# Performance work log

Measured on AMD Instinct MI355X. Metric: run time of the kernel, lower is better.

## Reference

```python
import jax, jax.numpy as jnp
import numpy as np

N_NODES = 100000
N_EDGES = 1600000
IN_F = 256
OUT_F = 64
ORDER = 3


def setup_inputs() -> dict:
    key = jax.random.key(0)
    k1, k2, k3, k4, k5 = jax.random.split(key, 5)
    x = jax.random.normal(k1, (N_NODES, IN_F), dtype=jnp.float32)
    # Linear params (torch nn.Linear: out = x @ W.T + b)
    W = jax.random.normal(k2, (OUT_F, IN_F), dtype=jnp.float32) * (1.0 / np.sqrt(IN_F))
    b = jnp.zeros((OUT_F,), dtype=jnp.float32)
    edge_src = jax.random.randint(k3, (N_EDGES,), 0, N_NODES, dtype=jnp.int32)
    edge_dst = jax.random.randint(k4, (N_EDGES,), 0, N_NODES, dtype=jnp.int32)
    # normalized-adjacency-like positive edge weights
    edge_weight = jax.random.uniform(k5, (N_EDGES,), dtype=jnp.float32) * 0.1
    return {"x": x, "W": W, "b": b, "edge_src": edge_src,
            "edge_dst": edge_dst, "edge_weight": edge_weight}


def reference(x, W, b, edge_src, edge_dst, edge_weight):
    # SGC: linear projection, then `order` hops of sparse adjacency matmul.
    out = x @ W.T + b  # [N, OUT_F]
    for _ in range(ORDER):
        # spmm: out[dst] += w_e * out[src] over all edges (COO)
        msgs = out[edge_src] * edge_weight[:, None]  # [E, OUT_F]
        out = jax.ops.segment_sum(msgs, edge_dst, num_segments=N_NODES)
    return out
```

## Files before the change

### kernel.cpp

```cpp
#include <hip/hip_runtime.h>

#define IN_F 256
#define OUT_F 64
#define BKT_BITS 8
#define BKT_NODES 256
#define BKT_CAP 6656
#define SRC_BITS 18
#define SRC_MASK 0x3FFFF
#define BIN_BLOCKS 256

typedef __attribute__((ext_vector_type(8))) short short8;
typedef __attribute__((ext_vector_type(4))) float floatx4;
typedef __attribute__((ext_vector_type(4))) int intx4;

static __device__ __forceinline__ short f2bf_rne(float f) {
    unsigned u = __float_as_uint(f);
    unsigned r = (u + 0x7fffu + ((u >> 16) & 1u)) >> 16;
    return (short)r;
}
static __device__ __forceinline__ float bf2f(short s) {
    return __uint_as_float(((unsigned)(unsigned short)s) << 16);
}
static __device__ __forceinline__ float bfu2f(unsigned short s) {
    return __uint_as_float(((unsigned)s) << 16);
}

__global__ __launch_bounds__(1024) void bin_kernel(const int* __restrict__ src,
                                                   const int* __restrict__ dst,
                                                   const float* __restrict__ w,
                                                   int* __restrict__ bkt_cnt,
                                                   int2* __restrict__ binned, int E, int nbkt) {
    __shared__ int h[512];
    int t = threadIdx.x;
    if (t < 512) h[t] = 0;
    __syncthreads();
    int ce = (E + BIN_BLOCKS - 1) / BIN_BLOCKS;
    int beg = blockIdx.x * ce;
    int end = min(E, beg + ce);
    for (int e = beg + t; e < end; e += 1024)
        atomicAdd(&h[__builtin_nontemporal_load(dst + e) >> BKT_BITS], 1);
    __syncthreads();
    int c = (t < 512) ? h[t] : 0;
    int r = 0;
    if (t < nbkt && c) r = atomicAdd(&bkt_cnt[t], c);
    __syncthreads();
    if (t < 512) h[t] = r;
    __syncthreads();
    for (int e = beg + t; e < end; e += 1024) {
        int d = dst[e];
        int bb = d >> BKT_BITS;
        int pos = atomicAdd(&h[bb], 1);
        binned[(size_t)bb * BKT_CAP + pos] =
            make_int2(((d & (BKT_NODES - 1)) << SRC_BITS) | src[e], __float_as_int(w[e]));
    }
}

__global__ __launch_bounds__(256) void build_bucket_kernel(const int2* __restrict__ binned,
                                                           const int* __restrict__ bkt_cnt,
                                                           int2* __restrict__ bego,
                                                           int2* __restrict__ edges,
                                                           int N) {
    __shared__ int h[BKT_NODES];
    __shared__ int ssum[256];
    int t = threadIdx.x;
    int b = blockIdx.x;
    h[t] = 0;
    __syncthreads();
    int cntb = bkt_cnt[b];
    const int2* bsrc = binned + (size_t)b * BKT_CAP;
    for (int e = t; e < cntb; e += 256) atomicAdd(&h[bsrc[e].x >> SRC_BITS], 1);
    __syncthreads();
    int c = h[t];
    int p = (c + 7) & ~7;
    ssum[t] = p;
    __syncthreads();
    for (int off = 1; off < 256; off <<= 1) {
        int v = (t >= off) ? ssum[t - off] : 0;
        __syncthreads();
        ssum[t] += v;
        __syncthreads();
    }
    int base = b * BKT_CAP + (t > 0 ? ssum[t - 1] : 0);
    int node = (b << BKT_BITS) + t;
    if (node < N) bego[node] = make_int2(base, base + p);
    __syncthreads();
    h[t] = base;
    __syncthreads();
    for (int e = t; e < cntb; e += 256) {
        int2 v = bsrc[e];
        int pos = atomicAdd(&h[v.x >> SRC_BITS], 1);
        edges[pos] = make_int2(v.x & SRC_MASK, v.y);
    }
    __syncthreads();
    for (int k = h[t]; k < base + p; ++k) edges[k] = make_int2(0, 0);
}

__global__ void prep_kernel(const float* __restrict__ W,
                            short* __restrict__ bh, short* __restrict__ bl,
                            int* __restrict__ bkt_cnt, int nbkt) {
    int blk = blockIdx.x;
    if (blk >= 8) {
        int i = (blk - 8) * 256 + threadIdx.x;
        if (i < nbkt) bkt_cnt[i] = 0;
        return;
    }
    int t = blk * 256 + threadIdx.x;
    int combo = t >> 6;
    int lane = t & 63;
    int s = combo >> 2;
    int tO = combo & 3;
    int n = 16 * tO + (lane & 15);
    int k0 = 32 * s + (lane >> 4) * 8;
    const float* src = W + (size_t)n * IN_F + k0;
    short* dh = bh + (size_t)t * 8;
    short* dl = bl + (size_t)t * 8;
#pragma unroll
    for (int j = 0; j < 8; ++j) {
        float v = src[j];
        short h = f2bf_rne(v);
        dh[j] = h;
        dl[j] = f2bf_rne(v - bf2f(h));
    }
}

__global__ __launch_bounds__(256) void gemm_kernel(const float* __restrict__ x,
                                                   const short8* __restrict__ bh,
                                                   const short8* __restrict__ bl,
                                                   const float* __restrict__ b,
                                                   unsigned short* __restrict__ obf, int N) {
    int lane = threadIdx.x & 63;
    int wid = threadIdx.x >> 6;
    int node0 = blockIdx.x * 64 + wid * 16;
    if (node0 >= N) return;
    if (node0 + 16 > N) node0 = N - 16;
    int m = lane & 15;
    int q = lane >> 4;

    const floatx4* xr = (const floatx4*)(x + (size_t)(node0 + m) * IN_F) + q * 2;

    floatx4 acc[4];
#pragma unroll
    for (int tO = 0; tO < 4; ++tO) acc[tO] = (floatx4){0.f, 0.f, 0.f, 0.f};

#pragma unroll
    for (int s = 0; s < 8; ++s) {
        floatx4 v0 = __builtin_nontemporal_load(xr + s * 8);
        floatx4 v1 = __builtin_nontemporal_load(xr + s * 8 + 1);
        float vv[8] = {v0[0], v0[1], v0[2], v0[3], v1[0], v1[1], v1[2], v1[3]};
        short8 ah, al;
#pragma unroll
        for (int j = 0; j < 8; ++j) {
            short h = f2bf_rne(vv[j]);
            ah[j] = h;
            al[j] = f2bf_rne(vv[j] - bf2f(h));
        }
#pragma unroll
        for (int tO = 0; tO < 4; ++tO) {
            short8 wh = bh[(s * 4 + tO) * 64 + lane];
            short8 wl = bl[(s * 4 + tO) * 64 + lane];
            acc[tO] = __builtin_amdgcn_mfma_f32_16x16x32_bf16(ah, wh, acc[tO], 0, 0, 0);
            acc[tO] = __builtin_amdgcn_mfma_f32_16x16x32_bf16(al, wh, acc[tO], 0, 0, 0);
            acc[tO] = __builtin_amdgcn_mfma_f32_16x16x32_bf16(ah, wl, acc[tO], 0, 0, 0);
        }
    }

#pragma unroll
    for (int tO = 0; tO < 4; ++tO) {
        float bias = b[16 * tO + m];
#pragma unroll
        for (int r = 0; r < 4; ++r) {
            obf[(size_t)(node0 + q * 4 + r) * OUT_F + 16 * tO + m] =
                (unsigned short)f2bf_rne(acc[tO][r] + bias);
        }
    }
}

#define GATHER_Q(NB)                                                                     \
    {                                                                                    \
        intx4 Q[NB];                                                                     \
        float v[2 * NB];                                                                 \
        _Pragma("unroll") for (int j = 0; j < NB; ++j) Q[j] = eq[j];                     \
        _Pragma("unroll") for (int j = 0; j < NB; ++j) {                                 \
            v[2 * j]     = bfu2f(in[(size_t)Q[j][0] * OUT_F + lane]);                    \
            v[2 * j + 1] = bfu2f(in[(size_t)Q[j][2] * OUT_F + lane]);                    \
        }                                                                                \
        _Pragma("unroll") for (int j = 0; j < NB; ++j) {                                 \
            acc = fmaf(__int_as_float(Q[j][1]), v[2 * j], acc);                          \
            acc = fmaf(__int_as_float(Q[j][3]), v[2 * j + 1], acc);                      \
        }                                                                                \
    }

static __device__ __forceinline__ float spmm_node(const int2* __restrict__ edges,
                                                  const unsigned short* __restrict__ in,
                                                  int lane, int e, int end) {
    float acc = 0.f;
    int deg = end - e;
    const intx4* eq = (const intx4*)(edges + e);
    if (deg == 16) {
        GATHER_Q(8)
    } else if (deg == 24) {
        GATHER_Q(12)
    } else if (deg == 8) {
        GATHER_Q(4)
    } else {
        while (e + 16 <= end) {
            GATHER_Q(8)
            e += 16;
            eq = (const intx4*)(edges + e);
        }
        if (e < end) {
            GATHER_Q(4)
        }
    }
    return acc;
}

template <bool OUT_BF>
__global__ __launch_bounds__(256) void spmm_kernel(const int2* __restrict__ bego,
                                                   const int2* __restrict__ edges,
                                                   const unsigned short* __restrict__ in,
                                                   void* __restrict__ outp, int N) {
    int gid = blockIdx.x * blockDim.x + threadIdx.x;
    int node = __builtin_amdgcn_readfirstlane(gid >> 6);
    int lane = threadIdx.x & 63;
    if (node >= N) return;
    int2 be = bego[node];
    float acc = spmm_node(edges, in, lane, be.x, be.y);
    if (OUT_BF) {
        unsigned short r = (unsigned short)f2bf_rne(acc);
        __builtin_nontemporal_store(r, (unsigned short*)outp + (size_t)node * OUT_F + lane);
    } else {
        __builtin_nontemporal_store(acc, (float*)outp + (size_t)node * OUT_F + lane);
    }
}

extern "C" void kernel_launch(void* const* d_in, const int* in_sizes, int n_in,
                              void* d_out, int out_size, void* d_ws, size_t ws_size,
                              hipStream_t stream) {
    const float* x = (const float*)d_in[0];
    const float* W = (const float*)d_in[1];
    const float* b = (const float*)d_in[2];
    const int* esrc = (const int*)d_in[3];
    const int* edst = (const int*)d_in[4];
    const float* ew = (const float*)d_in[5];
    float* out = (float*)d_out;

    int N = in_sizes[0] / IN_F;
    int E = in_sizes[3];
    int nbkt = (N + BKT_NODES - 1) >> BKT_BITS;

    char* ws = (char*)d_ws;
    size_t off = 0;
    unsigned short* bufA = (unsigned short*)(ws + off);  off += (size_t)N * OUT_F * 2;
    unsigned short* bufB = (unsigned short*)(ws + off);  off += (size_t)N * OUT_F * 2;
    int2* edges = (int2*)(ws + off);     off += (size_t)nbkt * BKT_CAP * sizeof(int2);
    int2* bego = (int2*)(ws + off);      off += (size_t)N * sizeof(int2);
    int* bkt_cnt = (int*)(ws + off);     off += 1024 * sizeof(int);
    short* bh = (short*)(ws + off);      off += 32 * 64 * 8 * sizeof(short);
    short* bl = (short*)(ws + off);      off += 32 * 64 * 8 * sizeof(short);
    int2* binned = (int2*)bufA;
    (void)ws_size; (void)n_in; (void)out_size;

    prep_kernel<<<10, 256, 0, stream>>>(W, bh, bl, bkt_cnt, nbkt);
    bin_kernel<<<BIN_BLOCKS, 1024, 0, stream>>>(esrc, edst, ew, bkt_cnt, binned, E, nbkt);
    build_bucket_kernel<<<nbkt, 256, 0, stream>>>(binned, bkt_cnt, bego, edges, N);

    gemm_kernel<<<(N + 63) / 64, 256, 0, stream>>>(x, (const short8*)bh, (const short8*)bl,
                                                   b, bufA, N);

    int spmm_blocks = (N * 64 + 255) / 256;
    spmm_kernel<true><<<spmm_blocks, 256, 0, stream>>>(bego, edges, bufA, bufB, N);
    spmm_kernel<true><<<spmm_blocks, 256, 0, stream>>>(bego, edges, bufB, bufA, N);
    spmm_kernel<false><<<spmm_blocks, 256, 0, stream>>>(bego, edges, bufA, out, N);
}
```

Before: 325.6 us.

## Fuse bucket build with GEMM launch and gather bf16 pairs in SpMM

Merges the bucket-build kernel and the projection GEMM into one launch with block ranges split by index, so the two independent stages run concurrently. This needs a separate binned buffer instead of aliasing bufA. The SpMM now has each half-wave take alternate edges and load packed pairs of bf16 features as 32-bit words, then combines the halves with a cross-lane shuffle. The goal is to halve the number of gather instructions and raise memory-level parallelism, at the cost of extra workspace and a reduction step.

```diff
diff --git a/kernel.cpp b/kernel.cpp
--- a/kernel.cpp
+++ b/kernel.cpp
@@ -11,7 +11,7 @@
 
 typedef __attribute__((ext_vector_type(8))) short short8;
 typedef __attribute__((ext_vector_type(4))) float floatx4;
-typedef __attribute__((ext_vector_type(4))) int intx4;
+typedef __attribute__((ext_vector_type(2))) float floatx2;
 
 static __device__ __forceinline__ short f2bf_rne(float f) {
     unsigned u = __float_as_uint(f);
@@ -20,9 +20,6 @@
 }
 static __device__ __forceinline__ float bf2f(short s) {
     return __uint_as_float(((unsigned)(unsigned short)s) << 16);
-}
-static __device__ __forceinline__ float bfu2f(unsigned short s) {
-    return __uint_as_float(((unsigned)s) << 16);
 }
 
 __global__ __launch_bounds__(1024) void bin_kernel(const int* __restrict__ src,
@@ -53,46 +50,6 @@
         binned[(size_t)bb * BKT_CAP + pos] =
             make_int2(((d & (BKT_NODES - 1)) << SRC_BITS) | src[e], __float_as_int(w[e]));
     }
-}
-
-__global__ __launch_bounds__(256) void build_bucket_kernel(const int2* __restrict__ binned,
-                                                           const int* __restrict__ bkt_cnt,
-                                                           int2* __restrict__ bego,
-                                                           int2* __restrict__ edges,
-                                                           int N) {
-    __shared__ int h[BKT_NODES];
-    __shared__ int ssum[256];
-    int t = threadIdx.x;
-    int b = blockIdx.x;
-    h[t] = 0;
-    __syncthreads();
-    int cntb = bkt_cnt[b];
-    const int2* bsrc = binned + (size_t)b * BKT_CAP;
-    for (int e = t; e < cntb; e += 256) atomicAdd(&h[bsrc[e].x >> SRC_BITS], 1);
-    __syncthreads();
-    int c = h[t];
-    int p = (c + 7) & ~7;
-    ssum[t] = p;
-    __syncthreads();
-    for (int off = 1; off < 256; off <<= 1) {
-        int v = (t >= off) ? ssum[t - off] : 0;
-        __syncthreads();
-        ssum[t] += v;
-        __syncthreads();
-    }
-    int base = b * BKT_CAP + (t > 0 ? ssum[t - 1] : 0);
-    int node = (b << BKT_BITS) + t;
-    if (node < N) bego[node] = make_int2(base, base + p);
-    __syncthreads();
-    h[t] = base;
-    __syncthreads();
-    for (int e = t; e < cntb; e += 256) {
-        int2 v = bsrc[e];
-        int pos = atomicAdd(&h[v.x >> SRC_BITS], 1);
-        edges[pos] = make_int2(v.x & SRC_MASK, v.y);
-    }
-    __syncthreads();
-    for (int k = h[t]; k < base + p; ++k) edges[k] = make_int2(0, 0);
 }
 
 __global__ void prep_kernel(const float* __restrict__ W,
@@ -123,14 +80,51 @@
     }
 }
 
-__global__ __launch_bounds__(256) void gemm_kernel(const float* __restrict__ x,
-                                                   const short8* __restrict__ bh,
-                                                   const short8* __restrict__ bl,
-                                                   const float* __restrict__ b,
-                                                   unsigned short* __restrict__ obf, int N) {
-    int lane = threadIdx.x & 63;
-    int wid = threadIdx.x >> 6;
-    int node0 = blockIdx.x * 64 + wid * 16;
+__global__ __launch_bounds__(256) void build_gemm_kernel(
+        const int2* __restrict__ binned, const int* __restrict__ bkt_cnt,
+        int2* __restrict__ bego, int2* __restrict__ edges, int nbkt,
+        const float* __restrict__ x, const short8* __restrict__ bh,
+        const short8* __restrict__ bl, const float* __restrict__ bias,
+        unsigned short* __restrict__ obf, int N) {
+    __shared__ int h[BKT_NODES];
+    __shared__ int ssum[256];
+    int t = threadIdx.x;
+    if ((int)blockIdx.x < nbkt) {
+        int bkt = blockIdx.x;
+        h[t] = 0;
+        __syncthreads();
+        int cntb = bkt_cnt[bkt];
+        const int2* bsrc = binned + (size_t)bkt * BKT_CAP;
+        for (int e = t; e < cntb; e += 256) atomicAdd(&h[bsrc[e].x >> SRC_BITS], 1);
+        __syncthreads();
+        int c = h[t];
+        int p = (c + 7) & ~7;
+        ssum[t] = p;
+        __syncthreads();
+        for (int off = 1; off < 256; off <<= 1) {
+            int v = (t >= off) ? ssum[t - off] : 0;
+            __syncthreads();
+            ssum[t] += v;
+            __syncthreads();
+        }
+        int base = bkt * BKT_CAP + (t > 0 ? ssum[t - 1] : 0);
+        int node = (bkt << BKT_BITS) + t;
+        if (node < N) bego[node] = make_int2(base, base + p);
+        __syncthreads();
+        h[t] = base;
+        __syncthreads();
+        for (int e = t; e < cntb; e += 256) {
+            int2 v = bsrc[e];
+            int pos = atomicAdd(&h[v.x >> SRC_BITS], 1);
+            edges[pos] = make_int2(v.x & SRC_MASK, v.y);
+        }
+        __syncthreads();
+        for (int k = h[t]; k < base + p; ++k) edges[k] = make_int2(0, 0);
+        return;
+    }
+    int lane = t & 63;
+    int wid = t >> 6;
+    int node0 = ((int)blockIdx.x - nbkt) * 64 + wid * 16;
     if (node0 >= N) return;
     if (node0 + 16 > N) node0 = N - 16;
     int m = lane & 15;
@@ -150,9 +144,9 @@
         short8 ah, al;
 #pragma unroll
         for (int j = 0; j < 8; ++j) {
-            short h = f2bf_rne(vv[j]);
-            ah[j] = h;
-            al[j] = f2bf_rne(vv[j] - bf2f(h));
+            short hh = f2bf_rne(vv[j]);
+            ah[j] = hh;
+            al[j] = f2bf_rne(vv[j] - bf2f(hh));
         }
 #pragma unroll
         for (int tO = 0; tO < 4; ++tO) {
@@ -166,54 +160,28 @@
 
 #pragma unroll
     for (int tO = 0; tO < 4; ++tO) {
-        float bias = b[16 * tO + m];
+        float bv = bias[16 * tO + m];
 #pragma unroll
         for (int r = 0; r < 4; ++r) {
             obf[(size_t)(node0 + q * 4 + r) * OUT_F + 16 * tO + m] =
-                (unsigned short)f2bf_rne(acc[tO][r] + bias);
-        }
-    }
-}
-
-#define GATHER_Q(NB)                                                                     \
+                (unsigned short)f2bf_rne(acc[tO][r] + bv);
+        }
+    }
+}
+
+#define GATHER_P(NS)                                                                     \
     {                                                                                    \
-        intx4 Q[NB];                                                                     \
-        float v[2 * NB];                                                                 \
-        _Pragma("unroll") for (int j = 0; j < NB; ++j) Q[j] = eq[j];                     \
-        _Pragma("unroll") for (int j = 0; j < NB; ++j) {                                 \
-            v[2 * j]     = bfu2f(in[(size_t)Q[j][0] * OUT_F + lane]);                    \
-            v[2 * j + 1] = bfu2f(in[(size_t)Q[j][2] * OUT_F + lane]);                    \
+        int2 Ev[NS];                                                                     \
+        unsigned dv[NS];                                                                 \
+        _Pragma("unroll") for (int j = 0; j < NS; ++j) Ev[j] = ed[2 * j + half];         \
+        _Pragma("unroll") for (int j = 0; j < NS; ++j)                                   \
+            dv[j] = *(const unsigned*)(in + (size_t)Ev[j].x * OUT_F + fl2);              \
+        _Pragma("unroll") for (int j = 0; j < NS; ++j) {                                 \
+            float wv = __int_as_float(Ev[j].y);                                          \
+            a0 = fmaf(wv, __uint_as_float(dv[j] << 16), a0);                             \
+            a1 = fmaf(wv, __uint_as_float(dv[j] & 0xFFFF0000u), a1);                     \
         }                                                                                \
-        _Pragma("unroll") for (int j = 0; j < NB; ++j) {                                 \
-            acc = fmaf(__int_as_float(Q[j][1]), v[2 * j], acc);                          \
-            acc = fmaf(__int_as_float(Q[j][3]), v[2 * j + 1], acc);                      \
-        }                                                                                \
-    }
-
-static __device__ __forceinline__ float spmm_node(const int2* __restrict__ edges,
-                                                  const unsigned short* __restrict__ in,
-                                                  int lane, int e, int end) {
-    float acc = 0.f;
-    int deg = end - e;
-    const intx4* eq = (const intx4*)(edges + e);
-    if (deg == 16) {
-        GATHER_Q(8)
-    } else if (deg == 24) {
-        GATHER_Q(12)
-    } else if (deg == 8) {
-        GATHER_Q(4)
-    } else {
-        while (e + 16 <= end) {
-            GATHER_Q(8)
-            e += 16;
-            eq = (const intx4*)(edges + e);
-        }
-        if (e < end) {
-            GATHER_Q(4)
-        }
-    }
-    return acc;
-}
+    }
 
 template <bool OUT_BF>
 __global__ __launch_bounds__(256) void spmm_kernel(const int2* __restrict__ bego,
@@ -224,13 +192,44 @@
     int node = __builtin_amdgcn_readfirstlane(gid >> 6);
     int lane = threadIdx.x & 63;
     if (node >= N) return;
+    int half = lane >> 5;
+    int fl2 = (lane & 31) * 2;
     int2 be = bego[node];
-    float acc = spmm_node(edges, in, lane, be.x, be.y);
-    if (OUT_BF) {
-        unsigned short r = (unsigned short)f2bf_rne(acc);
-        __builtin_nontemporal_store(r, (unsigned short*)outp + (size_t)node * OUT_F + lane);
+    int deg = be.y - be.x;
+    const int2* ed = edges + be.x;
+    float a0 = 0.f, a1 = 0.f;
+    if (deg == 16) {
+        GATHER_P(8)
+    } else if (deg == 24) {
+        GATHER_P(12)
+    } else if (deg == 8) {
+        GATHER_P(4)
     } else {
-        __builtin_nontemporal_store(acc, (float*)outp + (size_t)node * OUT_F + lane);
+        while (deg >= 32) {
+            GATHER_P(16)
+            ed += 32;
+            deg -= 32;
+        }
+        if (deg == 24) {
+            GATHER_P(12)
+        } else if (deg == 16) {
+            GATHER_P(8)
+        } else if (deg == 8) {
+            GATHER_P(4)
+        }
+    }
+    a0 += __shfl_xor(a0, 32);
+    a1 += __shfl_xor(a1, 32);
+    if (half == 0) {
+        int fl = lane & 31;
+        if (OUT_BF) {
+            unsigned pk = ((unsigned)(unsigned short)f2bf_rne(a1) << 16) |
+                          (unsigned)(unsigned short)f2bf_rne(a0);
+            __builtin_nontemporal_store(pk, (unsigned*)outp + (size_t)node * 32 + fl);
+        } else {
+            floatx2 r = {a0, a1};
+            __builtin_nontemporal_store(r, (floatx2*)outp + (size_t)node * 32 + fl);
+        }
     }
 }
 
@@ -254,19 +253,20 @@
     unsigned short* bufA = (unsigned short*)(ws + off);  off += (size_t)N * OUT_F * 2;
     unsigned short* bufB = (unsigned short*)(ws + off);  off += (size_t)N * OUT_F * 2;
     int2* edges = (int2*)(ws + off);     off += (size_t)nbkt * BKT_CAP * sizeof(int2);
+    int2* binned = (int2*)(ws + off);    off += (size_t)nbkt * BKT_CAP * sizeof(int2);
     int2* bego = (int2*)(ws + off);      off += (size_t)N * sizeof(int2);
     int* bkt_cnt = (int*)(ws + off);     off += 1024 * sizeof(int);
     short* bh = (short*)(ws + off);      off += 32 * 64 * 8 * sizeof(short);
     short* bl = (short*)(ws + off);      off += 32 * 64 * 8 * sizeof(short);
-    int2* binned = (int2*)bufA;
     (void)ws_size; (void)n_in; (void)out_size;
 
     prep_kernel<<<10, 256, 0, stream>>>(W, bh, bl, bkt_cnt, nbkt);
     bin_kernel<<<BIN_BLOCKS, 1024, 0, stream>>>(esrc, edst, ew, bkt_cnt, binned, E, nbkt);
-    build_bucket_kernel<<<nbkt, 256, 0, stream>>>(binned, bkt_cnt, bego, edges, N);
-
-    gemm_kernel<<<(N + 63) / 64, 256, 0, stream>>>(x, (const short8*)bh, (const short8*)bl,
-                                                   b, bufA, N);
+
+    int gemm_blocks = (N + 63) / 64;
+    build_gemm_kernel<<<nbkt + gemm_blocks, 256, 0, stream>>>(
+        binned, bkt_cnt, bego, edges, nbkt, x, (const short8*)bh, (const short8*)bl, b,
+        bufA, N);
 
     int spmm_blocks = (N * 64 + 255) / 256;
     spmm_kernel<true><<<spmm_blocks, 256, 0, stream>>>(bego, edges, bufA, bufB, N);
```

Measured after the change: 356.6 us. 9.5% more time.
